# Optimization experiments

Hardware: AMD Instinct MI355X
Metric: run time of the kernel (lower is better)

The kernel has to match this reference:

```python
import jax, jax.numpy as jnp
import numpy as np

EMBED_DIM = 1024
NUM_HEADS = 16
DIM_HEAD = EMBED_DIM // NUM_HEADS


def setup_inputs() -> dict:
    key = jax.random.key(0)
    ks = jax.random.split(key, 9)
    s = 1.0 / np.sqrt(EMBED_DIM)
    x = jax.random.normal(ks[0], (2, 2048, EMBED_DIM), dtype=jnp.float32)
    Wq = jax.random.uniform(ks[1], (EMBED_DIM, EMBED_DIM), jnp.float32, -s, s)
    bq = jax.random.uniform(ks[2], (EMBED_DIM,), jnp.float32, -s, s)
    Wk = jax.random.uniform(ks[3], (EMBED_DIM, EMBED_DIM), jnp.float32, -s, s)
    bk = jax.random.uniform(ks[4], (EMBED_DIM,), jnp.float32, -s, s)
    Wv = jax.random.uniform(ks[5], (EMBED_DIM, EMBED_DIM), jnp.float32, -s, s)
    bv = jax.random.uniform(ks[6], (EMBED_DIM,), jnp.float32, -s, s)
    Wo = jax.random.uniform(ks[7], (EMBED_DIM, EMBED_DIM), jnp.float32, -s, s)
    bo = jax.random.uniform(ks[8], (EMBED_DIM,), jnp.float32, -s, s)
    return {"x": x, "Wq": Wq, "bq": bq, "Wk": Wk, "bk": bk,
            "Wv": Wv, "bv": bv, "Wo": Wo, "bo": bo}


def reference(x, Wq, bq, Wk, bk, Wv, bv, Wo, bo):
    B, S, _ = x.shape
    # Linear layers (torch nn.Linear: x @ W.T + b), reshape to heads
    Q = (x @ Wq.T + bq).reshape(B, S, NUM_HEADS, DIM_HEAD)
    K = (x @ Wk.T + bk).reshape(B, S, NUM_HEADS, DIM_HEAD)
    V = (x @ Wv.T + bv).reshape(B, S, NUM_HEADS, DIM_HEAD)
    scores = jnp.einsum('bqhd,bkhd->bhqk', Q, K) / np.sqrt(DIM_HEAD)
    attn = jax.nn.softmax(scores, axis=-1)
    context = jnp.einsum('bhqk,bkhd->bqhd', attn, V).reshape(B, S, EMBED_DIM)
    return context @ Wo.T + bo
```

## Files before the change

kernel.cpp:

```cpp
#include <hip/hip_runtime.h>
#include <hip/hip_bf16.h>

#define SEQ   2048
#define EMB   1024
#define NHEAD 16
#define DHEAD 64
#define BATCH 2
#define MTOT  (BATCH*SEQ)
#define QT    128
#define KT    64
#define NTILE (SEQ/KT)

typedef __attribute__((ext_vector_type(8))) short s8v;
typedef __attribute__((ext_vector_type(4))) short s4v;
typedef __attribute__((ext_vector_type(4))) float f4v;

__device__ __forceinline__ short f2b(float f) {
    union { float fl; unsigned u; } v; v.fl = f;
    unsigned u = v.u;
    u = (u + 0x7fffu + ((u >> 16) & 1u)) >> 16;
    return (short)u;
}
__device__ __forceinline__ unsigned pk2(float a, float b) {
    union { __hip_bfloat162 h; unsigned u; } c;
    c.h = __float22bfloat162_rn(float2{a, b});
    return c.u;
}

#if __has_builtin(__builtin_amdgcn_exp2f)
__device__ __forceinline__ float exp2_fast(float x) { return __builtin_amdgcn_exp2f(x); }
#else
__device__ __forceinline__ float exp2_fast(float x) { return exp2f(x); }
#endif

__device__ __forceinline__ void pl32swap(unsigned &a, unsigned &b) {
    asm("v_permlane32_swap_b32 %0, %1" : "+v"(a), "+v"(b));
}
__device__ __forceinline__ void pl16swap(unsigned &a, unsigned &b) {
    asm("v_permlane16_swap_b32 %0, %1" : "+v"(a), "+v"(b));
}

__device__ __forceinline__ void bar_lds() {
    asm volatile("s_waitcnt lgkmcnt(0)\n\ts_barrier" ::: "memory");
}

__device__ __forceinline__ void gl_lds16(const short* g, short* l) {
    __builtin_amdgcn_global_load_lds(
        (const __attribute__((address_space(1))) void*)g,
        (__attribute__((address_space(3))) void*)l, 16, 0, 0);
}

__global__ __launch_bounds__(256)
void cvt_swz(const float* __restrict__ s0, const float* __restrict__ s1,
             const float* __restrict__ s2, const float* __restrict__ s3,
             const float* __restrict__ s4,
             short* __restrict__ d0, short* __restrict__ d1,
             short* __restrict__ d2, short* __restrict__ d3,
             short* __restrict__ d4)
{
    const int seg = blockIdx.y;
    const float* s = seg == 0 ? s0 : seg == 1 ? s1 : seg == 2 ? s2 : seg == 3 ? s3 : s4;
    short*       d = seg == 0 ? d0 : seg == 1 ? d1 : seg == 2 ? d2 : seg == 3 ? d3 : d4;
    const int nchunk = (seg == 0 ? MTOT * EMB : EMB * EMB) / 8;
    const int stride = gridDim.x * 256;
    for (int i = blockIdx.x * 256 + threadIdx.x; i < nchunk; i += stride) {
        const int row = i >> 7;
        const int c   = i & 127;
        const float4 v0 = *(const float4*)(s + (size_t)i * 8);
        const float4 v1 = *(const float4*)(s + (size_t)i * 8 + 4);
        union { unsigned uu[4]; s8v s8; } o;
        o.uu[0] = pk2(v0.x, v0.y);
        o.uu[1] = pk2(v0.z, v0.w);
        o.uu[2] = pk2(v1.x, v1.y);
        o.uu[3] = pk2(v1.z, v1.w);
        const int cp = (c & ~7) | ((c & 7) ^ (row & 7));
        *(s8v*)(d + (size_t)row * EMB + cp * 8) = o.s8;
    }
}

template<int NT, bool FUSED3>
__global__ __launch_bounds__(256, 3)
void gemm_bb3(const short* __restrict__ A,
              const short* __restrict__ W0, const short* __restrict__ W1, const short* __restrict__ W2,
              const float* __restrict__ B0, const float* __restrict__ B1, const float* __restrict__ B2,
              void* __restrict__ C0, void* __restrict__ C1, void* __restrict__ C2)
{
    constexpr int JN = NT / 32;
    const int K = EMB, N = EMB;
    const int ntiles = EMB / NT;

    const int L   = blockIdx.x + gridDim.x * blockIdx.y;
    const int xcd = L & 7;
    const int s   = L >> 3;
    constexpr int XW = FUSED3 ? 12 : 8;
    const int x = (xcd & 1) * XW + s / 8;
    const int y = (xcd >> 1) * 8 + (s & 7);

    const int mat = x / ntiles;
    const int n0  = (x % ntiles) * NT;
    const int m0  = y * 128;
    const short* W  = (mat == 0) ? W0 : (mat == 1 ? W1 : W2);
    const float* Bi = (mat == 0) ? B0 : (mat == 1 ? B1 : B2);
    void*        C  = (mat == 0) ? C0 : (mat == 1 ? C1 : C2);
    const float qscale = (FUSED3 && mat == 0) ? 0.18033688f : 1.0f;

    const int tid  = threadIdx.x;
    const int lane = tid & 63;
    const int wave = tid >> 6;
    const int quad = lane >> 4;
    const int l16  = lane & 15;
    const int l8   = l16 & 7;
    const int wm   = wave >> 1;
    const int wn   = wave & 1;

    f4v acc[4][JN] = {};

    const int srow = lane >> 3;
    const int scol = (lane & 7) * 8;

    if constexpr (FUSED3) {
        __shared__ __align__(16) short As[128 * 64];
        __shared__ __align__(16) short Ws[NT * 64];

        for (int k0 = 0; k0 < K; k0 += 64) {
            #pragma unroll
            for (int p = 0; p < 4; ++p) {
                const int rbase = wave * 32 + p * 8;
                gl_lds16(A + (size_t)(m0 + rbase + srow) * K + k0 + scol,
                         As + rbase * 64);
            }
            #pragma unroll
            for (int p = 0; p < NT / 32; ++p) {
                const int rbase = wave * (NT / 4) + p * 8;
                gl_lds16(W + (size_t)(n0 + rbase + srow) * K + k0 + scol,
                         Ws + rbase * 64);
            }
            __syncthreads();

            #pragma unroll
            for (int kk = 0; kk < 2; ++kk) {
                const int slot = ((kk * 4 + quad) ^ l8) * 8;
                s8v af[4], wf[JN];
                #pragma unroll
                for (int i = 0; i < 4; ++i)
                    af[i] = *(const s8v*)(As + (wm * 64 + i * 16 + l16) * 64 + slot);
                #pragma unroll
                for (int j = 0; j < JN; ++j)
                    wf[j] = *(const s8v*)(Ws + (wn * (NT / 2) + j * 16 + l16) * 64 + slot);
                #pragma unroll
                for (int i = 0; i < 4; ++i)
                    #pragma unroll
                    for (int j = 0; j < JN; ++j)
                        acc[i][j] = __builtin_amdgcn_mfma_f32_16x16x32_bf16(
                            af[i], wf[j], acc[i][j], 0, 0, 0);
            }
            __syncthreads();
        }

        #pragma unroll
        for (int j = 0; j < JN; ++j) {
            const int n = n0 + wn * (NT / 2) + j * 16 + l16;
            const float bv = Bi[n];
            #pragma unroll
            for (int i = 0; i < 4; ++i) {
                const int mb = m0 + wm * 64 + i * 16 + quad * 4;
                if (mat == 2) {
                    const int bb = mb >> 11, ss = mb & 2047;
                    s4v ov;
                    #pragma unroll
                    for (int rr = 0; rr < 4; ++rr) ov[rr] = f2b(acc[i][j][rr] + bv);
                    *(s4v*)((short*)C + ((size_t)(bb * 1024 + n)) * SEQ + ss) = ov;
                } else {
                    #pragma unroll
                    for (int rr = 0; rr < 4; ++rr)
                        ((short*)C)[(size_t)(mb + rr) * N + n] = f2b((acc[i][j][rr] + bv) * qscale);
                }
            }
        }
    } else {
        __shared__ __align__(16) short As[2][128 * 64];
        __shared__ __align__(16) short Ws[2][NT * 64];

        #pragma unroll
        for (int p = 0; p < 4; ++p) {
            const int rbase = wave * 32 + p * 8;
            gl_lds16(A + (size_t)(m0 + rbase + srow) * K + scol, As[0] + rbase * 64);
        }
        #pragma unroll
        for (int p = 0; p < NT / 32; ++p) {
            const int rbase = wave * (NT / 4) + p * 8;
            gl_lds16(W + (size_t)(n0 + rbase + srow) * K + scol, Ws[0] + rbase * 64);
        }

        for (int t = 0; t < K / 64; ++t) {
            const int buf = t & 1;
            __syncthreads();
            if (t + 1 < K / 64) {
                const int k1 = (t + 1) * 64;
                #pragma unroll
                for (int p = 0; p < 4; ++p) {
                    const int rbase = wave * 32 + p * 8;
                    gl_lds16(A + (size_t)(m0 + rbase + srow) * K + k1 + scol,
                             As[buf ^ 1] + rbase * 64);
                }
                #pragma unroll
                for (int p = 0; p < NT / 32; ++p) {
                    const int rbase = wave * (NT / 4) + p * 8;
                    gl_lds16(W + (size_t)(n0 + rbase + srow) * K + k1 + scol,
                             Ws[buf ^ 1] + rbase * 64);
                }
            }
            const short* AsB = As[buf];
            const short* WsB = Ws[buf];

            #pragma unroll
            for (int kk = 0; kk < 2; ++kk) {
                const int slot = ((kk * 4 + quad) ^ l8) * 8;
                s8v af[4], wf[JN];
                #pragma unroll
                for (int i = 0; i < 4; ++i)
                    af[i] = *(const s8v*)(AsB + (wm * 64 + i * 16 + l16) * 64 + slot);
                #pragma unroll
                for (int j = 0; j < JN; ++j)
                    wf[j] = *(const s8v*)(WsB + (wn * (NT / 2) + j * 16 + l16) * 64 + slot);
                #pragma unroll
                for (int i = 0; i < 4; ++i)
                    #pragma unroll
                    for (int j = 0; j < JN; ++j)
                        acc[i][j] = __builtin_amdgcn_mfma_f32_16x16x32_bf16(
                            af[i], wf[j], acc[i][j], 0, 0, 0);
            }
        }

        #pragma unroll
        for (int j = 0; j < JN; ++j) {
            const int n = n0 + wn * (NT / 2) + j * 16 + l16;
            const float bv = Bi[n];
            #pragma unroll
            for (int i = 0; i < 4; ++i) {
                const int mb = m0 + wm * 64 + i * 16 + quad * 4;
                #pragma unroll
                for (int rr = 0; rr < 4; ++rr)
                    ((float*)C)[(size_t)(mb + rr) * N + n] = acc[i][j][rr] + bv;
            }
        }
    }
}

__global__ __launch_bounds__(512, 4)
void attn_mfma7(const short* Q, const short* __restrict__ Kg,
                const short* __restrict__ Vt, short* O)
{
    const int i    = blockIdx.x;
    const int xcd  = i & 7;
    const int slot = i >> 3;
    const int combo = xcd * 4 + (slot >> 4);
    const int qb = slot & 15;
    const int h  = combo & 15;
    const int b  = combo >> 4;
    const int q0 = qb * QT;

    const int tid  = threadIdx.x;
    const int lane = tid & 63;
    const int wave = tid >> 6;
    const int quad = lane >> 4;
    const int l16  = lane & 15;
    const int l8   = l16 & 7;

    __shared__ __align__(16) short Ks[2][64 * 64];
    __shared__ __align__(16) short Vs[2][64 * 64];

    s8v qf[2];
    #pragma unroll
    for (int kk = 0; kk < 2; ++kk)
        qf[kk] = *(const s8v*)(Q + (size_t)(b * SEQ + q0 + wave * 16 + l16) * EMB
                                 + h * DHEAD + kk * 32 + quad * 8);

    f4v oacc[4] = {};
    f4v sacc    = {};
    s8v onef;
    #pragma unroll
    for (int e = 0; e < 8; ++e) onef[e] = (short)0x3F80;

    const int r = lane >> 3, c = lane & 7;
    const int sc8 = (c ^ r) * 8;
    const bool isK = wave < 4;
    const int wrow = (wave & 3) * 16;
    const size_t kbase = (size_t)(b * SEQ) * EMB + h * DHEAD;
    const size_t vbase = (size_t)((b * NHEAD + h) * DHEAD) * SEQ;
    const short* gsrc = isK ? Kg + kbase + (size_t)(wrow + r) * EMB + sc8
                            : Vt + vbase + (size_t)(wrow + r) * SEQ + sc8;
    const size_t gstep8 = isK ? (size_t)8 * EMB : (size_t)8 * SEQ;
    const size_t tstep  = isK ? (size_t)KT * EMB : (size_t)KT;
    short* const lbase  = (isK ? (short*)Ks : (short*)Vs) + wrow * 64;

    gl_lds16(gsrc,          lbase);
    gl_lds16(gsrc + gstep8, lbase + 8 * 64);
    const short* gnext = gsrc + tstep;

    for (int t = 0; t < NTILE; ++t) {
        const int buf = t & 1;
        __syncthreads();
        if (t + 1 < NTILE) {
            short* ldst = lbase + (buf ^ 1) * (64 * 64);
            gl_lds16(gnext,          ldst);
            gl_lds16(gnext + gstep8, ldst + 8 * 64);
            gnext += tstep;
        }
        const short* KsB = Ks[buf];
        const short* VsB = Vs[buf];

        f4v sc[4] = {};
        #pragma unroll
        for (int kk = 0; kk < 2; ++kk) {
            const int ko = ((kk * 4 + quad) ^ l8) * 8;
            s8v kf[4];
            #pragma unroll
            for (int j = 0; j < 4; ++j)
                kf[j] = *(const s8v*)(KsB + (j * 16 + l16) * 64 + ko);
            #pragma unroll
            for (int j = 0; j < 4; ++j)
                sc[j] = __builtin_amdgcn_mfma_f32_16x16x32_bf16(
                    kf[j], qf[kk], sc[j], 0, 0, 0);
        }

        unsigned u[4][2];
        #pragma unroll
        for (int j = 0; j < 4; ++j) {
            u[j][0] = pk2(exp2_fast(sc[j][0]), exp2_fast(sc[j][1]));
            u[j][1] = pk2(exp2_fast(sc[j][2]), exp2_fast(sc[j][3]));
        }

        #pragma unroll
        for (int r2 = 0; r2 < 2; ++r2) {
            pl32swap(u[0][r2], u[1][r2]);
            pl32swap(u[2][r2], u[3][r2]);
            pl16swap(u[0][r2], u[1][r2]);
            pl16swap(u[2][r2], u[3][r2]);
        }
        union { unsigned uu[4]; s8v s; } pfa, pfb;
        pfa.uu[0] = u[0][0]; pfa.uu[1] = u[0][1]; pfa.uu[2] = u[1][0]; pfa.uu[3] = u[1][1];
        pfb.uu[0] = u[2][0]; pfb.uu[1] = u[2][1]; pfb.uu[2] = u[3][0]; pfb.uu[3] = u[3][1];

        #pragma unroll
        for (int kk = 0; kk < 2; ++kk) {
            const s8v pf = kk ? pfb.s : pfa.s;
            sacc = __builtin_amdgcn_mfma_f32_16x16x32_bf16(onef, pf, sacc, 0, 0, 0);
            const int ko = ((kk * 4 + quad) ^ l8) * 8;
            #pragma unroll
            for (int j = 0; j < 4; ++j) {
                const s8v vf = *(const s8v*)(VsB + (j * 16 + l16) * 64 + ko);
                oacc[j] = __builtin_amdgcn_mfma_f32_16x16x32_bf16(
                    vf, pf, oacc[j], 0, 0, 0);
            }
        }
    }

    const float inv = 1.0f / sacc[0];

    __syncthreads();
    short* Os = (short*)Ks;
    #pragma unroll
    for (int j = 0; j < 4; ++j) {
        union { unsigned uu[2]; s4v s; } ov;
        ov.uu[0] = pk2(oacc[j][0] * inv, oacc[j][1] * inv);
        ov.uu[1] = pk2(oacc[j][2] * inv, oacc[j][3] * inv);
        const int pc = ((j * 2 + (quad >> 1)) ^ l8) * 8 + (quad & 1) * 4;
        *(s4v*)(Os + (wave * 16 + l16) * 64 + pc) = ov.s;
    }
    bar_lds();

    const int row = tid >> 2;
    const int cb  = (tid & 3) * 2;
    #pragma unroll
    for (int c4 = 0; c4 < 2; ++c4) {
        const int pcc = cb + c4;
        const s8v tt = *(const s8v*)(Os + row * 64 + pcc * 8);
        *(s8v*)(O + (size_t)(b * SEQ + q0 + row) * EMB + h * DHEAD + pcc * 8) = tt;
    }
}

extern "C" void kernel_launch(void* const* d_in, const int* in_sizes, int n_in,
                              void* d_out, int out_size, void* d_ws, size_t ws_size,
                              hipStream_t stream)
{
    const float* x  = (const float*)d_in[0];
    const float* Wq = (const float*)d_in[1];
    const float* bq = (const float*)d_in[2];
    const float* Wk = (const float*)d_in[3];
    const float* bk = (const float*)d_in[4];
    const float* Wv = (const float*)d_in[5];
    const float* bv = (const float*)d_in[6];
    const float* Wo = (const float*)d_in[7];
    const float* bo = (const float*)d_in[8];
    float* out = (float*)d_out;

    short* xb  = (short*)d_ws;
    short* Wqb = xb  + (size_t)MTOT * EMB;
    short* Wkb = Wqb + (size_t)EMB * EMB;
    short* Wvb = Wkb + (size_t)EMB * EMB;
    short* Wob = Wvb + (size_t)EMB * EMB;
    short* Qw  = Wob + (size_t)EMB * EMB;
    short* Kw  = Qw  + (size_t)MTOT * EMB;
    short* Vtw = Kw  + (size_t)MTOT * EMB;

    cvt_swz<<<dim3(512, 5), 256, 0, stream>>>(x, Wq, Wk, Wv, Wo,
                                              xb, Wqb, Wkb, Wvb, Wob);

    gemm_bb3<128, true><<<dim3(24, 32), 256, 0, stream>>>(
        xb, Wqb, Wkb, Wvb, bq, bk, bv, Qw, Kw, Vtw);

    attn_mfma7<<<dim3(BATCH * NHEAD * (SEQ / QT)), 512, 0, stream>>>(Qw, Kw, Vtw, Qw);

    gemm_bb3<64, false><<<dim3(16, 32), 256, 0, stream>>>(
        Qw, Wob, Wob, Wob, bo, bo, bo, out, out, out);
}
```

Baseline: 178.5 us.

## Fuse Q/K/V projections per block to share the activation tile

Replaces the QKV GEMM, where each block computed one 128x128 tile of a single projection, with a kernel where each block computes a 128x64 tile of all three projections. Each x tile loaded into shared memory is reused against the Wq, Wk and Wv tiles. This is meant to cut redundant activation loads and give more MFMA work per shared-memory stage. In exchange it triples the accumulator registers, lowers the occupancy target to 2 blocks per CU, and reduces the grid to 512 blocks. The output projection is split into its own non-templated kernel with the same logic as before.

```diff
diff --git a/kernel.cpp b/kernel.cpp
--- a/kernel.cpp
+++ b/kernel.cpp
@@ -78,31 +78,24 @@
     }
 }
 
-template<int NT, bool FUSED3>
-__global__ __launch_bounds__(256, 3)
-void gemm_bb3(const short* __restrict__ A,
+__global__ __launch_bounds__(256, 2)
+void gemm_qkv(const short* __restrict__ A,
               const short* __restrict__ W0, const short* __restrict__ W1, const short* __restrict__ W2,
               const float* __restrict__ B0, const float* __restrict__ B1, const float* __restrict__ B2,
-              void* __restrict__ C0, void* __restrict__ C1, void* __restrict__ C2)
+              short* __restrict__ Cq, short* __restrict__ Ck, short* __restrict__ Cv)
 {
-    constexpr int JN = NT / 32;
     const int K = EMB, N = EMB;
-    const int ntiles = EMB / NT;
 
     const int L   = blockIdx.x + gridDim.x * blockIdx.y;
     const int xcd = L & 7;
     const int s   = L >> 3;
-    constexpr int XW = FUSED3 ? 12 : 8;
-    const int x = (xcd & 1) * XW + s / 8;
-    const int y = (xcd >> 1) * 8 + (s & 7);
-
-    const int mat = x / ntiles;
-    const int n0  = (x % ntiles) * NT;
+    const int x   = (xcd & 1) * 8 + (s >> 3);
+    const int y   = (xcd >> 1) * 8 + (s & 7);
+    const int n0  = x * 64;
     const int m0  = y * 128;
-    const short* W  = (mat == 0) ? W0 : (mat == 1 ? W1 : W2);
-    const float* Bi = (mat == 0) ? B0 : (mat == 1 ? B1 : B2);
-    void*        C  = (mat == 0) ? C0 : (mat == 1 ? C1 : C2);
-    const float qscale = (FUSED3 && mat == 0) ? 0.18033688f : 1.0f;
+
+    __shared__ __align__(16) short As[128 * 64];
+    __shared__ __align__(16) short Ws[3][64 * 64];
 
     const int tid  = threadIdx.x;
     const int lane = tid & 63;
@@ -113,136 +106,168 @@
     const int wm   = wave >> 1;
     const int wn   = wave & 1;
 
-    f4v acc[4][JN] = {};
+    f4v acc[3][4][2] = {};
 
     const int srow = lane >> 3;
     const int scol = (lane & 7) * 8;
 
-    if constexpr (FUSED3) {
-        __shared__ __align__(16) short As[128 * 64];
-        __shared__ __align__(16) short Ws[NT * 64];
-
-        for (int k0 = 0; k0 < K; k0 += 64) {
-            #pragma unroll
-            for (int p = 0; p < 4; ++p) {
-                const int rbase = wave * 32 + p * 8;
-                gl_lds16(A + (size_t)(m0 + rbase + srow) * K + k0 + scol,
-                         As + rbase * 64);
-            }
-            #pragma unroll
-            for (int p = 0; p < NT / 32; ++p) {
-                const int rbase = wave * (NT / 4) + p * 8;
-                gl_lds16(W + (size_t)(n0 + rbase + srow) * K + k0 + scol,
-                         Ws + rbase * 64);
-            }
-            __syncthreads();
-
-            #pragma unroll
-            for (int kk = 0; kk < 2; ++kk) {
-                const int slot = ((kk * 4 + quad) ^ l8) * 8;
-                s8v af[4], wf[JN];
+    for (int k0 = 0; k0 < K; k0 += 64) {
+        #pragma unroll
+        for (int p = 0; p < 4; ++p) {
+            const int rbase = wave * 32 + p * 8;
+            gl_lds16(A + (size_t)(m0 + rbase + srow) * K + k0 + scol,
+                     As + rbase * 64);
+        }
+        #pragma unroll
+        for (int p = 0; p < 2; ++p) {
+            const int rbase = wave * 16 + p * 8;
+            const size_t off = (size_t)(n0 + rbase + srow) * K + k0 + scol;
+            gl_lds16(W0 + off, Ws[0] + rbase * 64);
+            gl_lds16(W1 + off, Ws[1] + rbase * 64);
+            gl_lds16(W2 + off, Ws[2] + rbase * 64);
+        }
+        __syncthreads();
+
+        #pragma unroll
+        for (int kk = 0; kk < 2; ++kk) {
+            const int slot = ((kk * 4 + quad) ^ l8) * 8;
+            s8v af[4], wf[3][2];
+            #pragma unroll
+            for (int i = 0; i < 4; ++i)
+                af[i] = *(const s8v*)(As + (wm * 64 + i * 16 + l16) * 64 + slot);
+            #pragma unroll
+            for (int m = 0; m < 3; ++m)
                 #pragma unroll
-                for (int i = 0; i < 4; ++i)
-                    af[i] = *(const s8v*)(As + (wm * 64 + i * 16 + l16) * 64 + slot);
-                #pragma unroll
-                for (int j = 0; j < JN; ++j)
-                    wf[j] = *(const s8v*)(Ws + (wn * (NT / 2) + j * 16 + l16) * 64 + slot);
+                for (int j = 0; j < 2; ++j)
+                    wf[m][j] = *(const s8v*)(Ws[m] + (wn * 32 + j * 16 + l16) * 64 + slot);
+            #pragma unroll
+            for (int m = 0; m < 3; ++m)
                 #pragma unroll
                 for (int i = 0; i < 4; ++i)
                     #pragma unroll
-                    for (int j = 0; j < JN; ++j)
-                        acc[i][j] = __builtin_amdgcn_mfma_f32_16x16x32_bf16(
-                            af[i], wf[j], acc[i][j], 0, 0, 0);
+                    for (int j = 0; j < 2; ++j)
+                        acc[m][i][j] = __builtin_amdgcn_mfma_f32_16x16x32_bf16(
+                            af[i], wf[m][j], acc[m][i][j], 0, 0, 0);
+        }
+        __syncthreads();
+    }
+
+    #pragma unroll
+    for (int j = 0; j < 2; ++j) {
+        const int n = n0 + wn * 32 + j * 16 + l16;
+        const float bq_ = B0[n], bk_ = B1[n], bv_ = B2[n];
+        #pragma unroll
+        for (int i = 0; i < 4; ++i) {
+            const int mb = m0 + wm * 64 + i * 16 + quad * 4;
+            #pragma unroll
+            for (int rr = 0; rr < 4; ++rr)
+                Cq[(size_t)(mb + rr) * N + n] = f2b((acc[0][i][j][rr] + bq_) * 0.18033688f);
+            #pragma unroll
+            for (int rr = 0; rr < 4; ++rr)
+                Ck[(size_t)(mb + rr) * N + n] = f2b(acc[1][i][j][rr] + bk_);
+            const int bb = mb >> 11, ss = mb & 2047;
+            s4v ov;
+            #pragma unroll
+            for (int rr = 0; rr < 4; ++rr) ov[rr] = f2b(acc[2][i][j][rr] + bv_);
+            *(s4v*)(Cv + ((size_t)(bb * 1024 + n)) * SEQ + ss) = ov;
+        }
+    }
+}
+
+__global__ __launch_bounds__(256, 3)
+void gemm_out(const short* __restrict__ A, const short* __restrict__ W,
+              const float* __restrict__ Bi, float* __restrict__ C)
+{
+    constexpr int NT = 64;
+    constexpr int JN = NT / 32;
+    const int K = EMB, N = EMB;
+
+    const int L   = blockIdx.x + gridDim.x * blockIdx.y;
+    const int xcd = L & 7;
+    const int s   = L >> 3;
+    const int x   = (xcd & 1) * 8 + (s >> 3);
+    const int y   = (xcd >> 1) * 8 + (s & 7);
+    const int n0  = x * NT;
+    const int m0  = y * 128;
+
+    const int tid  = threadIdx.x;
+    const int lane = tid & 63;
+    const int wave = tid >> 6;
+    const int quad = lane >> 4;
+    const int l16  = lane & 15;
+    const int l8   = l16 & 7;
+    const int wm   = wave >> 1;
+    const int wn   = wave & 1;
+
+    f4v acc[4][JN] = {};
+
+    const int srow = lane >> 3;
+    const int scol = (lane & 7) * 8;
+
+    __shared__ __align__(16) short As[2][128 * 64];
+    __shared__ __align__(16) short Ws[2][NT * 64];
+
+    #pragma unroll
+    for (int p = 0; p < 4; ++p) {
+        const int rbase = wave * 32 + p * 8;
+        gl_lds16(A + (size_t)(m0 + rbase + srow) * K + scol, As[0] + rbase * 64);
+    }
+    #pragma unroll
+    for (int p = 0; p < NT / 32; ++p) {
+        const int rbase = wave * (NT / 4) + p * 8;
+        gl_lds16(W + (size_t)(n0 + rbase + srow) * K + scol, Ws[0] + rbase * 64);
+    }
+
+    for (int t = 0; t < K / 64; ++t) {
+        const int buf = t & 1;
+        __syncthreads();
+        if (t + 1 < K / 64) {
+            const int k1 = (t + 1) * 64;
+            #pragma unroll
+            for (int p = 0; p < 4; ++p) {
+                const int rbase = wave * 32 + p * 8;
+                gl_lds16(A + (size_t)(m0 + rbase + srow) * K + k1 + scol,
+                         As[buf ^ 1] + rbase * 64);
             }
-            __syncthreads();
-        }
-
-        #pragma unroll
-        for (int j = 0; j < JN; ++j) {
-            const int n = n0 + wn * (NT / 2) + j * 16 + l16;
-            const float bv = Bi[n];
-            #pragma unroll
-            for (int i = 0; i < 4; ++i) {
-                const int mb = m0 + wm * 64 + i * 16 + quad * 4;
-                if (mat == 2) {
-                    const int bb = mb >> 11, ss = mb & 2047;
-                    s4v ov;
-                    #pragma unroll
-                    for (int rr = 0; rr < 4; ++rr) ov[rr] = f2b(acc[i][j][rr] + bv);
-                    *(s4v*)((short*)C + ((size_t)(bb * 1024 + n)) * SEQ + ss) = ov;
-                } else {
-                    #pragma unroll
-                    for (int rr = 0; rr < 4; ++rr)
-                        ((short*)C)[(size_t)(mb + rr) * N + n] = f2b((acc[i][j][rr] + bv) * qscale);
-                }
+            #pragma unroll
+            for (int p = 0; p < NT / 32; ++p) {
+                const int rbase = wave * (NT / 4) + p * 8;
+                gl_lds16(W + (size_t)(n0 + rbase + srow) * K + k1 + scol,
+                         Ws[buf ^ 1] + rbase * 64);
             }
         }
-    } else {
-        __shared__ __align__(16) short As[2][128 * 64];
-        __shared__ __align__(16) short Ws[2][NT * 64];
-
-        #pragma unroll
-        for (int p = 0; p < 4; ++p) {
-            const int rbase = wave * 32 + p * 8;
-            gl_lds16(A + (size_t)(m0 + rbase + srow) * K + scol, As[0] + rbase * 64);
-        }
-        #pragma unroll
-        for (int p = 0; p < NT / 32; ++p) {
-            const int rbase = wave * (NT / 4) + p * 8;
-            gl_lds16(W + (size_t)(n0 + rbase + srow) * K + scol, Ws[0] + rbase * 64);
-        }
-
-        for (int t = 0; t < K / 64; ++t) {
-            const int buf = t & 1;
-            __syncthreads();
-            if (t + 1 < K / 64) {
-                const int k1 = (t + 1) * 64;
-                #pragma unroll
-                for (int p = 0; p < 4; ++p) {
-                    const int rbase = wave * 32 + p * 8;
-                    gl_lds16(A + (size_t)(m0 + rbase + srow) * K + k1 + scol,
-                             As[buf ^ 1] + rbase * 64);
-                }
-                #pragma unroll
-                for (int p = 0; p < NT / 32; ++p) {
-                    const int rbase = wave * (NT / 4) + p * 8;
-                    gl_lds16(W + (size_t)(n0 + rbase + srow) * K + k1 + scol,
-                             Ws[buf ^ 1] + rbase * 64);
-                }
-            }
-            const short* AsB = As[buf];
-            const short* WsB = Ws[buf];
-
-            #pragma unroll
-            for (int kk = 0; kk < 2; ++kk) {
-                const int slot = ((kk * 4 + quad) ^ l8) * 8;
-                s8v af[4], wf[JN];
-                #pragma unroll
-                for (int i = 0; i < 4; ++i)
-                    af[i] = *(const s8v*)(AsB + (wm * 64 + i * 16 + l16) * 64 + slot);
+        const short* AsB = As[buf];
+        const short* WsB = Ws[buf];
+
+        #pragma unroll
+        for (int kk = 0; kk < 2; ++kk) {
+            const int slot = ((kk * 4 + quad) ^ l8) * 8;
+            s8v af[4], wf[JN];
+            #pragma unroll
+            for (int i = 0; i < 4; ++i)
+                af[i] = *(const s8v*)(AsB + (wm * 64 + i * 16 + l16) * 64 + slot);
+            #pragma unroll
+            for (int j = 0; j < JN; ++j)
+                wf[j] = *(const s8v*)(WsB + (wn * (NT / 2) + j * 16 + l16) * 64 + slot);
+            #pragma unroll
+            for (int i = 0; i < 4; ++i)
                 #pragma unroll
                 for (int j = 0; j < JN; ++j)
-                    wf[j] = *(const s8v*)(WsB + (wn * (NT / 2) + j * 16 + l16) * 64 + slot);
-                #pragma unroll
-                for (int i = 0; i < 4; ++i)
-                    #pragma unroll
-                    for (int j = 0; j < JN; ++j)
-                        acc[i][j] = __builtin_amdgcn_mfma_f32_16x16x32_bf16(
-                            af[i], wf[j], acc[i][j], 0, 0, 0);
-            }
-        }
-
-        #pragma unroll
-        for (int j = 0; j < JN; ++j) {
-            const int n = n0 + wn * (NT / 2) + j * 16 + l16;
-            const float bv = Bi[n];
-            #pragma unroll
-            for (int i = 0; i < 4; ++i) {
-                const int mb = m0 + wm * 64 + i * 16 + quad * 4;
-                #pragma unroll
-                for (int rr = 0; rr < 4; ++rr)
-                    ((float*)C)[(size_t)(mb + rr) * N + n] = acc[i][j][rr] + bv;
-            }
+                    acc[i][j] = __builtin_amdgcn_mfma_f32_16x16x32_bf16(
+                        af[i], wf[j], acc[i][j], 0, 0, 0);
+        }
+    }
+
+    #pragma unroll
+    for (int j = 0; j < JN; ++j) {
+        const int n = n0 + wn * (NT / 2) + j * 16 + l16;
+        const float bv = Bi[n];
+        #pragma unroll
+        for (int i = 0; i < 4; ++i) {
+            const int mb = m0 + wm * 64 + i * 16 + quad * 4;
+            #pragma unroll
+            for (int rr = 0; rr < 4; ++rr)
+                C[(size_t)(mb + rr) * N + n] = acc[i][j][rr] + bv;
         }
     }
 }
@@ -407,11 +432,10 @@
     cvt_swz<<<dim3(512, 5), 256, 0, stream>>>(x, Wq, Wk, Wv, Wo,
                                               xb, Wqb, Wkb, Wvb, Wob);
 
-    gemm_bb3<128, true><<<dim3(24, 32), 256, 0, stream>>>(
+    gemm_qkv<<<dim3(16, 32), 256, 0, stream>>>(
         xb, Wqb, Wkb, Wvb, bq, bk, bv, Qw, Kw, Vtw);
 
     attn_mfma7<<<dim3(BATCH * NHEAD * (SEQ / QT)), 512, 0, stream>>>(Qw, Kw, Vtw, Qw);
 
-    gemm_bb3<64, false><<<dim3(16, 32), 256, 0, stream>>>(
-        Qw, Wob, Wob, Wob, bo, bo, bo, out, out, out);
-}
+    gemm_out<<<dim3(16, 32), 256, 0, stream>>>(Qw, Wob, bo, out);
+}
```

Result: no change. 180.8 us (+1.3%).
